# Kernel tuning notes

Measured on AMD Instinct MI355X. Metric: run time of the kernel, lower is better.

The kernel has to match this reference:

```python
import jax, jax.numpy as jnp
import numpy as np

N = 8192
D_FEAT = 1024
EPS = 1e-8


def setup_inputs() -> dict:
    key = jax.random.key(0)
    k1, k2 = jax.random.split(key)
    features = jax.random.normal(k1, (N, D_FEAT), dtype=jnp.float32)
    # nonnegative adjacency-like matrix (weights in [0,1))
    Mat = jax.random.uniform(k2, (N, N), dtype=jnp.float32)
    index = jnp.arange(N, dtype=jnp.int64)
    return {"features": features, "Mat": Mat, "index": index}


def reference(features, Mat, index):
    # Symmetric degree normalization: D^-1/2 A D^-1/2
    rowsum = Mat.sum(axis=1)                      # [N]
    d_inv_sqrt = (rowsum + EPS) ** -0.5
    d_inv_sqrt = jnp.where(jnp.isinf(d_inv_sqrt), 0.0, d_inv_sqrt)
    A_norm = Mat * d_inv_sqrt[:, None] * d_inv_sqrt[None, :]
    # GCN aggregation: spmm equivalent
    out = A_norm @ features                       # [N, d]
    # new_features[index] = out; rows not in index keep original features
    new_features = features.at[index].set(out)
    return new_features
```

## Files before the change

kernel.cpp:

```cpp
#include <hip/hip_runtime.h>


#define N_NODES 8192
#define D_FEAT  1024
#define GCN_EPS 1e-8f

typedef __attribute__((ext_vector_type(8))) short bf16x8;
typedef __attribute__((ext_vector_type(4))) float f32x4;
typedef __attribute__((ext_vector_type(4))) float f32x4v;
typedef __attribute__((ext_vector_type(4))) unsigned short u16x4v;

__device__ inline unsigned short f2bf(float x) {
  unsigned u = __float_as_uint(x);
  u += 0x7FFFu + ((u >> 16) & 1u);
  return (unsigned short)(u >> 16);
}

__device__ inline void async_copy16(const void* g, void* l) {
  __builtin_amdgcn_global_load_lds(
      (const __attribute__((address_space(1))) void*)g,
      (__attribute__((address_space(3))) void*)l,
      16, 0, 0);
}

__global__ __launch_bounds__(256) void rowsum_convert(
    const float* __restrict__ Mat, unsigned short* __restrict__ Abf,
    float* __restrict__ dvec) {
  const int row = blockIdx.x;
  const int tid = threadIdx.x;
  const f32x4v* src = (const f32x4v*)(Mat + (size_t)row * N_NODES);
  u16x4v* dst = (u16x4v*)(Abf + (size_t)row * N_NODES);
  float s = 0.f;
#pragma unroll
  for (int i = 0; i < 8; ++i) {
    int idx = tid + i * 256;
    f32x4v v = __builtin_nontemporal_load(&src[idx]);
    s += (v.x + v.y) + (v.z + v.w);
    u16x4v o;
    o.x = f2bf(v.x); o.y = f2bf(v.y); o.z = f2bf(v.z); o.w = f2bf(v.w);
    __builtin_nontemporal_store(o, &dst[idx]);
  }
#pragma unroll
  for (int off = 32; off > 0; off >>= 1) s += __shfl_down(s, off);
  __shared__ float red[4];
  const int lane = tid & 63, wave = tid >> 6;
  if (lane == 0) red[wave] = s;
  __syncthreads();
  if (tid == 0) {
    float t = (red[0] + red[1]) + (red[2] + red[3]);
    dvec[row] = 1.0f / sqrtf(t + GCN_EPS);
  }
}

__global__ __launch_bounds__(256) void scale_transpose(
    const float* __restrict__ F, const float* __restrict__ dvec,
    unsigned short* __restrict__ Fst) {
  __shared__ float tile[32][33];
  const int tx = threadIdx.x, ty = threadIdx.y;
  const int n0 = blockIdx.x * 32;
  const int j0 = blockIdx.y * 32;
#pragma unroll
  for (int i = 0; i < 4; ++i) {
    int j = j0 + ty + i * 8;
    tile[ty + i * 8][tx] = dvec[j] * F[(size_t)j * D_FEAT + n0 + tx];
  }
  __syncthreads();
#pragma unroll
  for (int i = 0; i < 4; ++i) {
    int n = n0 + ty + i * 8;
    Fst[(size_t)n * N_NODES + j0 + tx] = f2bf(tile[tx][ty + i * 8]);
  }
}

__global__ __launch_bounds__(256, 4) void gemm_bt(
    const unsigned short* __restrict__ A,
    const unsigned short* __restrict__ Bt,
    const float* __restrict__ dvec,
    float* __restrict__ C) {
  const int K = N_NODES;
  __shared__ __align__(16) unsigned short As[64 * 32];
  __shared__ __align__(16) unsigned short Bs[128 * 32];

  const int tid = threadIdx.x;
  const int wave = tid >> 6, lane = tid & 63;
  const int tileM = blockIdx.y * 64, tileN = blockIdx.x * 128;
  const int wm = (wave >> 1) * 32, wn = (wave & 1) * 64;
  const int lrow = lane & 15, quad = lane >> 4;

  const int cA = tid;
  const int cB0 = tid, cB1 = tid + 256;
  const unsigned short* gA  = A  + (size_t)(tileM + (cA  >> 2)) * K + (cA  & 3) * 8;
  const unsigned short* gB0 = Bt + (size_t)(tileN + (cB0 >> 2)) * K + (cB0 & 3) * 8;
  const unsigned short* gB1 = Bt + (size_t)(tileN + (cB1 >> 2)) * K + (cB1 & 3) * 8;
  unsigned short* lA  = &As[wave * 512];
  unsigned short* lB0 = &Bs[wave * 512];
  unsigned short* lB1 = &Bs[2048 + wave * 512];

  f32x4 acc[2][4] = {};

  for (int k0 = 0; k0 < K; k0 += 32) {
    __syncthreads();
    async_copy16(gA + k0, lA);
    async_copy16(gB0 + k0, lB0);
    async_copy16(gB1 + k0, lB1);
    __syncthreads();

    bf16x8 af[2], bfr[4];
#pragma unroll
    for (int mi = 0; mi < 2; ++mi)
      af[mi] = *(const bf16x8*)&As[(wm + mi * 16 + lrow) * 32 + quad * 8];
#pragma unroll
    for (int ni = 0; ni < 4; ++ni)
      bfr[ni] = *(const bf16x8*)&Bs[(wn + ni * 16 + lrow) * 32 + quad * 8];
#pragma unroll
    for (int mi = 0; mi < 2; ++mi)
#pragma unroll
      for (int ni = 0; ni < 4; ++ni)
        acc[mi][ni] = __builtin_amdgcn_mfma_f32_16x16x32_bf16(
            af[mi], bfr[ni], acc[mi][ni], 0, 0, 0);
  }

#pragma unroll
  for (int mi = 0; mi < 2; ++mi) {
#pragma unroll
    for (int r = 0; r < 4; ++r) {
      int row = tileM + wm + mi * 16 + quad * 4 + r;
      float dv = dvec[row];
#pragma unroll
      for (int ni = 0; ni < 4; ++ni) {
        int col = tileN + wn + ni * 16 + lrow;
        C[(size_t)row * D_FEAT + col] = dv * acc[mi][ni][r];
      }
    }
  }
}

extern "C" void kernel_launch(void* const* d_in, const int* in_sizes, int n_in,
                              void* d_out, int out_size, void* d_ws, size_t ws_size,
                              hipStream_t stream) {
  const float* F   = (const float*)d_in[0];
  const float* Mat = (const float*)d_in[1];
  float* out = (float*)d_out;

  char* ws = (char*)d_ws;
  float* dvec = (float*)ws;
  unsigned short* Fst = (unsigned short*)(ws + 32768);
  unsigned short* Abf = (unsigned short*)(ws + 32768 + (size_t)D_FEAT * N_NODES * 2);

  rowsum_convert<<<N_NODES, 256, 0, stream>>>(Mat, Abf, dvec);
  scale_transpose<<<dim3(D_FEAT / 32, N_NODES / 32), dim3(32, 8), 0, stream>>>(F, dvec, Fst);
  gemm_bt<<<dim3(D_FEAT / 128, N_NODES / 64), 256, 0, stream>>>(Abf, Fst, dvec, out);
}
```

Before: 614.7 us.

## Enlarge GEMM tile to 128x128, vectorize transpose, drop nontemporal hints

The GEMM block tile grows from 64x128 to 128x128, so each wave computes a 64x64 output with 16 MFMA accumulators. This raises reuse of the A/B tiles in LDS and halves the number of blocks. The scale-transpose kernel now works on 64x64 tiles with float4 loads and 4-wide bf16 stores. The rowsum conversion pass switches from nontemporal to ordinary loads and stores, so its bf16 copy of A may stay in cache for the GEMM. The larger tile costs more registers and drops the occupancy hint of 4 blocks per CU, leaving fewer blocks to hide the single-buffered load latency.

```diff
diff --git a/kernel.cpp b/kernel.cpp
--- a/kernel.cpp
+++ b/kernel.cpp
@@ -7,8 +7,7 @@
 
 typedef __attribute__((ext_vector_type(8))) short bf16x8;
 typedef __attribute__((ext_vector_type(4))) float f32x4;
-typedef __attribute__((ext_vector_type(4))) float f32x4v;
-typedef __attribute__((ext_vector_type(4))) unsigned short u16x4v;
+typedef __attribute__((ext_vector_type(4))) unsigned short u16x4;
 
 __device__ inline unsigned short f2bf(float x) {
   unsigned u = __float_as_uint(x);
@@ -28,17 +27,17 @@
     float* __restrict__ dvec) {
   const int row = blockIdx.x;
   const int tid = threadIdx.x;
-  const f32x4v* src = (const f32x4v*)(Mat + (size_t)row * N_NODES);
-  u16x4v* dst = (u16x4v*)(Abf + (size_t)row * N_NODES);
+  const f32x4* src = (const f32x4*)(Mat + (size_t)row * N_NODES);
+  u16x4* dst = (u16x4*)(Abf + (size_t)row * N_NODES);
   float s = 0.f;
 #pragma unroll
   for (int i = 0; i < 8; ++i) {
     int idx = tid + i * 256;
-    f32x4v v = __builtin_nontemporal_load(&src[idx]);
+    f32x4 v = src[idx];
     s += (v.x + v.y) + (v.z + v.w);
-    u16x4v o;
+    u16x4 o;
     o.x = f2bf(v.x); o.y = f2bf(v.y); o.z = f2bf(v.z); o.w = f2bf(v.w);
-    __builtin_nontemporal_store(o, &dst[idx]);
+    dst[idx] = o;
   }
 #pragma unroll
   for (int off = 32; off > 0; off >>= 1) s += __shfl_down(s, off);
@@ -55,65 +54,78 @@
 __global__ __launch_bounds__(256) void scale_transpose(
     const float* __restrict__ F, const float* __restrict__ dvec,
     unsigned short* __restrict__ Fst) {
-  __shared__ float tile[32][33];
-  const int tx = threadIdx.x, ty = threadIdx.y;
-  const int n0 = blockIdx.x * 32;
-  const int j0 = blockIdx.y * 32;
+  __shared__ float tile[64][65];
+  const int t = threadIdx.x;
+  const int n0 = blockIdx.x * 64;
+  const int j0 = blockIdx.y * 64;
+  const int jr = t >> 4;
+  const int c = t & 15;
 #pragma unroll
   for (int i = 0; i < 4; ++i) {
-    int j = j0 + ty + i * 8;
-    tile[ty + i * 8][tx] = dvec[j] * F[(size_t)j * D_FEAT + n0 + tx];
+    int jj = jr + 16 * i;
+    float dv = dvec[j0 + jj];
+    f32x4 v = *(const f32x4*)(F + (size_t)(j0 + jj) * D_FEAT + n0 + c * 4);
+    tile[jj][c * 4 + 0] = v.x * dv;
+    tile[jj][c * 4 + 1] = v.y * dv;
+    tile[jj][c * 4 + 2] = v.z * dv;
+    tile[jj][c * 4 + 3] = v.w * dv;
   }
   __syncthreads();
 #pragma unroll
   for (int i = 0; i < 4; ++i) {
-    int n = n0 + ty + i * 8;
-    Fst[(size_t)n * N_NODES + j0 + tx] = f2bf(tile[tx][ty + i * 8]);
+    int nn = jr + 16 * i;
+    u16x4 o;
+    o.x = f2bf(tile[c * 4 + 0][nn]);
+    o.y = f2bf(tile[c * 4 + 1][nn]);
+    o.z = f2bf(tile[c * 4 + 2][nn]);
+    o.w = f2bf(tile[c * 4 + 3][nn]);
+    *(u16x4*)(Fst + (size_t)(n0 + nn) * N_NODES + j0 + c * 4) = o;
   }
 }
 
-__global__ __launch_bounds__(256, 4) void gemm_bt(
+__global__ __launch_bounds__(256) void gemm_bt(
     const unsigned short* __restrict__ A,
     const unsigned short* __restrict__ Bt,
     const float* __restrict__ dvec,
     float* __restrict__ C) {
   const int K = N_NODES;
-  __shared__ __align__(16) unsigned short As[64 * 32];
+  __shared__ __align__(16) unsigned short As[128 * 32];
   __shared__ __align__(16) unsigned short Bs[128 * 32];
 
   const int tid = threadIdx.x;
   const int wave = tid >> 6, lane = tid & 63;
-  const int tileM = blockIdx.y * 64, tileN = blockIdx.x * 128;
-  const int wm = (wave >> 1) * 32, wn = (wave & 1) * 64;
+  const int tileM = blockIdx.y * 128, tileN = blockIdx.x * 128;
+  const int wm = (wave >> 1) * 64, wn = (wave & 1) * 64;
   const int lrow = lane & 15, quad = lane >> 4;
 
-  const int cA = tid;
-  const int cB0 = tid, cB1 = tid + 256;
-  const unsigned short* gA  = A  + (size_t)(tileM + (cA  >> 2)) * K + (cA  & 3) * 8;
-  const unsigned short* gB0 = Bt + (size_t)(tileN + (cB0 >> 2)) * K + (cB0 & 3) * 8;
-  const unsigned short* gB1 = Bt + (size_t)(tileN + (cB1 >> 2)) * K + (cB1 & 3) * 8;
-  unsigned short* lA  = &As[wave * 512];
+  const unsigned short* gA0 = A + (size_t)(tileM + (tid >> 2)) * K + (tid & 3) * 8;
+  const unsigned short* gA1 = A + (size_t)(tileM + 64 + (tid >> 2)) * K + (tid & 3) * 8;
+  const unsigned short* gB0 = Bt + (size_t)(tileN + (tid >> 2)) * K + (tid & 3) * 8;
+  const unsigned short* gB1 = Bt + (size_t)(tileN + 64 + (tid >> 2)) * K + (tid & 3) * 8;
+  unsigned short* lA0 = &As[wave * 512];
+  unsigned short* lA1 = &As[2048 + wave * 512];
   unsigned short* lB0 = &Bs[wave * 512];
   unsigned short* lB1 = &Bs[2048 + wave * 512];
 
-  f32x4 acc[2][4] = {};
+  f32x4 acc[4][4] = {};
 
   for (int k0 = 0; k0 < K; k0 += 32) {
     __syncthreads();
-    async_copy16(gA + k0, lA);
+    async_copy16(gA0 + k0, lA0);
+    async_copy16(gA1 + k0, lA1);
     async_copy16(gB0 + k0, lB0);
     async_copy16(gB1 + k0, lB1);
     __syncthreads();
 
-    bf16x8 af[2], bfr[4];
+    bf16x8 af[4], bfr[4];
 #pragma unroll
-    for (int mi = 0; mi < 2; ++mi)
+    for (int mi = 0; mi < 4; ++mi)
       af[mi] = *(const bf16x8*)&As[(wm + mi * 16 + lrow) * 32 + quad * 8];
 #pragma unroll
     for (int ni = 0; ni < 4; ++ni)
       bfr[ni] = *(const bf16x8*)&Bs[(wn + ni * 16 + lrow) * 32 + quad * 8];
 #pragma unroll
-    for (int mi = 0; mi < 2; ++mi)
+    for (int mi = 0; mi < 4; ++mi)
 #pragma unroll
       for (int ni = 0; ni < 4; ++ni)
         acc[mi][ni] = __builtin_amdgcn_mfma_f32_16x16x32_bf16(
@@ -121,7 +133,7 @@
   }
 
 #pragma unroll
-  for (int mi = 0; mi < 2; ++mi) {
+  for (int mi = 0; mi < 4; ++mi) {
 #pragma unroll
     for (int r = 0; r < 4; ++r) {
       int row = tileM + wm + mi * 16 + quad * 4 + r;
@@ -138,7 +150,7 @@
 extern "C" void kernel_launch(void* const* d_in, const int* in_sizes, int n_in,
                               void* d_out, int out_size, void* d_ws, size_t ws_size,
                               hipStream_t stream) {
-  const float* F   = (const float*)d_in[0];
+  const float* F = (const float*)d_in[0];
   const float* Mat = (const float*)d_in[1];
   float* out = (float*)d_out;
 
@@ -148,6 +160,6 @@
   unsigned short* Abf = (unsigned short*)(ws + 32768 + (size_t)D_FEAT * N_NODES * 2);
 
   rowsum_convert<<<N_NODES, 256, 0, stream>>>(Mat, Abf, dvec);
-  scale_transpose<<<dim3(D_FEAT / 32, N_NODES / 32), dim3(32, 8), 0, stream>>>(F, dvec, Fst);
-  gemm_bt<<<dim3(D_FEAT / 128, N_NODES / 64), 256, 0, stream>>>(Abf, Fst, dvec, out);
+  scale_transpose<<<dim3(D_FEAT / 64, N_NODES / 64), 256, 0, stream>>>(F, dvec, Fst);
+  gemm_bt<<<dim3(D_FEAT / 128, N_NODES / 128), 256, 0, stream>>>(Abf, Fst, dvec, out);
 }
```

New measurement: 615.3 us. No clear change (+0.1%).
